# Optimization experiments

Hardware: AMD Instinct MI355X
Metric: run time of the kernel (lower is better)

The kernel has to match this reference:

```python
import jax, jax.numpy as jnp
import numpy as np

B, S, D = 1, 2048, 2048
H, DH, DHID, DKER = 16, 128, 128, 64
EPS = 1e-6

def _gelu(x):
    return jax.nn.gelu(x, approximate=False)  # torch F.gelu default is exact erf

def setup_inputs() -> dict:
    key = jax.random.key(0)
    ks = jax.random.split(key, 12)
    inp = {
        'q': jax.random.normal(ks[0], (B, S, D), jnp.float32),
        'k': jax.random.normal(ks[1], (B, S, D), jnp.float32),
        'v': jax.random.normal(ks[2], (B, S, D), jnp.float32),
        'lr_attn_mask': jax.random.randint(ks[3], (1, 1, S, S), 0, 2) > 0,
        'sparse_norms_lse': jax.random.normal(ks[4], (B, H, S, 1), jnp.float32),
        'sparse_attn_weights': jax.random.normal(ks[5], (B, H, S, S), jnp.float32) * 0.1,
        'kernel_q_mat1': jax.random.normal(ks[6], (H, DH, DHID), jnp.float32) * 0.05,
        'kernel_k_mat1': jax.random.normal(ks[7], (H, DH, DHID), jnp.float32) * 0.05,
        'kernel_q_mat2': jax.random.normal(ks[8], (H, DHID, DKER), jnp.float32) * 0.05,
        'kernel_k_mat2': jax.random.normal(ks[9], (H, DHID, DKER), jnp.float32) * 0.05,
        'interaction_k': jax.random.normal(ks[10], (H, DKER, DKER), jnp.float32) * 0.05,
        'scalingD': jnp.ones((1, H, 1, DKER), jnp.float32) * 1e-4,
        'scalingD2': jnp.ones((1, H, 1, DKER), jnp.float32) * 1e-4,
    }
    return inp

def reference(q, k, v, lr_attn_mask, sparse_norms_lse, sparse_attn_weights,
              kernel_q_mat1, kernel_k_mat1, kernel_q_mat2, kernel_k_mat2,
              interaction_k, scalingD, scalingD2):
    b, s, d = q.shape
    dh = d // H
    # [B,S,D] -> [B,H,S,dh]
    q = q.reshape(b, s, H, dh).transpose(0, 2, 1, 3)
    k = k.reshape(b, s, H, dh).transpose(0, 2, 1, 3)
    v = v.reshape(b, s, H, dh).transpose(0, 2, 1, 3)
    # per-head kernel feature maps (dropout is identity, p=0.0)
    q = _gelu(jnp.einsum('bhsd,hde->bhse', q, kernel_q_mat1))
    q = _gelu(jnp.einsum('bhsd,hde->bhse', q, kernel_q_mat2))
    k = _gelu(jnp.einsum('bhsd,hde->bhse', k, kernel_k_mat1))
    k = jnp.abs(scalingD) * _gelu(jnp.einsum('bhsd,hde->bhse', k, kernel_k_mat2))
    k = k + jnp.einsum('bhse,hef->bhsf', k, interaction_k) * scalingD2
    # low-rank kernelized scores: [B,H,S,S]
    out = jnp.einsum('bhse,bhte->bhst', jnp.abs(q), jnp.abs(k))
    mask = lr_attn_mask  # bool, broadcasts over [B,H,S,S]
    out = jnp.where(mask, out, 0.0)
    lr_norms_lse = jnp.log(out.sum(axis=-1, keepdims=True) + EPS)
    norm_factor_lse = jnp.logaddexp(lr_norms_lse, sparse_norms_lse)
    # log-domain merge of low-rank and sparse scores
    out = jnp.where(mask, jnp.log(out + EPS), sparse_attn_weights)
    out = jnp.exp(out - norm_factor_lse)
    out = jnp.einsum('bhst,bhtd->bhsd', out, v)
    return out.transpose(0, 2, 1, 3).reshape(b, s, d)
```

## Files before the change

kernel.cpp:

```cpp
#include <hip/hip_runtime.h>
#include <math.h>

#define S 2048
#define DD 2048
#define NH 16
#define DH 128
#define DHID 128
#define DKER 64
#define EPSF 1e-6f

typedef __attribute__((ext_vector_type(8))) short bf16x8;
typedef __attribute__((ext_vector_type(4))) float f32x4;

__device__ __forceinline__ float gelu_f(float x) {
    return 0.5f * x * (1.0f + erff(x * 0.7071067811865475f));
}

__device__ __forceinline__ ushort f2b(float x) {
    uint32_t u = __float_as_uint(x);
    uint32_t r = (u + 0x7FFFu + ((u >> 16) & 1u)) >> 16;
    return (ushort)r;
}

__global__ __launch_bounds__(256) void k_mlp1(const float* __restrict__ X,
                                              const float* __restrict__ Wall,
                                              float* __restrict__ Y) {
    const int h = blockIdx.y;
    const int s0 = blockIdx.x * 64;
    const int tid = threadIdx.x;
    const int ty = tid >> 4, tx = tid & 15;
    __shared__ float Xs[64][20];
    __shared__ float Ws[16][128];
    const float* Wh = Wall + h * DH * DHID;
    float acc[4][8] = {};

    const int lr = tid >> 2, lc = tid & 3;
    const int wr = tid >> 5, wc = tid & 31;
    for (int kc = 0; kc < 8; ++kc) {
        *(float4*)(&Xs[lr][lc * 4]) =
            *(const float4*)(X + (size_t)(s0 + lr) * DD + h * DH + kc * 16 + lc * 4);
        *(float4*)(&Ws[wr][wc * 4]) =
            *(const float4*)(Wh + (kc * 16 + wr) * DHID + wc * 4);
        *(float4*)(&Ws[wr + 8][wc * 4]) =
            *(const float4*)(Wh + (kc * 16 + wr + 8) * DHID + wc * 4);
        __syncthreads();
        #pragma unroll
        for (int kk = 0; kk < 16; ++kk) {
            float a[4];
            #pragma unroll
            for (int i = 0; i < 4; ++i) a[i] = Xs[ty * 4 + i][kk];
            float4 b0 = *(const float4*)(&Ws[kk][tx * 8]);
            float4 b1 = *(const float4*)(&Ws[kk][tx * 8 + 4]);
            #pragma unroll
            for (int i = 0; i < 4; ++i) {
                acc[i][0] += a[i] * b0.x; acc[i][1] += a[i] * b0.y;
                acc[i][2] += a[i] * b0.z; acc[i][3] += a[i] * b0.w;
                acc[i][4] += a[i] * b1.x; acc[i][5] += a[i] * b1.y;
                acc[i][6] += a[i] * b1.z; acc[i][7] += a[i] * b1.w;
            }
        }
        __syncthreads();
    }
    float* Yp = Y + ((size_t)h * S + s0) * DHID;
    #pragma unroll
    for (int i = 0; i < 4; ++i) {
        float4 o0, o1;
        o0.x = gelu_f(acc[i][0]); o0.y = gelu_f(acc[i][1]);
        o0.z = gelu_f(acc[i][2]); o0.w = gelu_f(acc[i][3]);
        o1.x = gelu_f(acc[i][4]); o1.y = gelu_f(acc[i][5]);
        o1.z = gelu_f(acc[i][6]); o1.w = gelu_f(acc[i][7]);
        *(float4*)(Yp + (ty * 4 + i) * DHID + tx * 8) = o0;
        *(float4*)(Yp + (ty * 4 + i) * DHID + tx * 8 + 4) = o1;
    }
}

__global__ __launch_bounds__(256) void k_mlp2_q(const float* __restrict__ Y1,
                                                const float* __restrict__ Wall,
                                                ushort* __restrict__ Q2) {
    const int h = blockIdx.y;
    const int s0 = blockIdx.x * 64;
    const int tid = threadIdx.x;
    const int ty = tid >> 4, tx = tid & 15;
    __shared__ float Ys[64][20];
    __shared__ float Ws[16][64];
    const float* Wh = Wall + h * DHID * DKER;
    float acc[4][4] = {};
    const int lr = tid >> 2, lc = tid & 3;
    const int wr = tid >> 4, wc = tid & 15;
    for (int kc = 0; kc < 8; ++kc) {
        *(float4*)(&Ys[lr][lc * 4]) =
            *(const float4*)(Y1 + ((size_t)h * S + s0 + lr) * DHID + kc * 16 + lc * 4);
        *(float4*)(&Ws[wr][wc * 4]) =
            *(const float4*)(Wh + (kc * 16 + wr) * DKER + wc * 4);
        __syncthreads();
        #pragma unroll
        for (int kk = 0; kk < 16; ++kk) {
            float4 b = *(const float4*)(&Ws[kk][tx * 4]);
            #pragma unroll
            for (int i = 0; i < 4; ++i) {
                float a = Ys[ty * 4 + i][kk];
                acc[i][0] += a * b.x; acc[i][1] += a * b.y;
                acc[i][2] += a * b.z; acc[i][3] += a * b.w;
            }
        }
        __syncthreads();
    }
    ushort* Qp = Q2 + ((size_t)h * S + s0) * DKER;
    #pragma unroll
    for (int i = 0; i < 4; ++i) {
        ushort4 o;
        o.x = f2b(fabsf(gelu_f(acc[i][0]))); o.y = f2b(fabsf(gelu_f(acc[i][1])));
        o.z = f2b(fabsf(gelu_f(acc[i][2]))); o.w = f2b(fabsf(gelu_f(acc[i][3])));
        *(ushort4*)(Qp + (ty * 4 + i) * DKER + tx * 4) = o;
    }
}

__global__ __launch_bounds__(256) void k_mlp2_k(const float* __restrict__ Y1,
                                                const float* __restrict__ Wall,
                                                const float* __restrict__ Ikall,
                                                const float* __restrict__ sD,
                                                const float* __restrict__ sD2,
                                                ushort* __restrict__ K3) {
    const int h = blockIdx.y;
    const int s0 = blockIdx.x * 64;
    const int tid = threadIdx.x;
    const int ty = tid >> 4, tx = tid & 15;
    __shared__ float Ys[64][20];
    __shared__ float Ws[16][64];
    __shared__ float K2s[64][68];
    __shared__ float Iks[64][64];
    const float* Wh = Wall + h * DHID * DKER;
    const float* Ikh = Ikall + h * DKER * DKER;
    #pragma unroll
    for (int it = 0; it < 4; ++it) {
        int idx = it * 256 + tid;
        int r = idx >> 4, c = idx & 15;
        *(float4*)(&Iks[r][c * 4]) = *(const float4*)(Ikh + r * DKER + c * 4);
    }
    float acc[4][4] = {};
    const int lr = tid >> 2, lc = tid & 3;
    const int wr = tid >> 4, wc = tid & 15;
    for (int kc = 0; kc < 8; ++kc) {
        *(float4*)(&Ys[lr][lc * 4]) =
            *(const float4*)(Y1 + ((size_t)h * S + s0 + lr) * DHID + kc * 16 + lc * 4);
        *(float4*)(&Ws[wr][wc * 4]) =
            *(const float4*)(Wh + (kc * 16 + wr) * DKER + wc * 4);
        __syncthreads();
        #pragma unroll
        for (int kk = 0; kk < 16; ++kk) {
            float4 b = *(const float4*)(&Ws[kk][tx * 4]);
            #pragma unroll
            for (int i = 0; i < 4; ++i) {
                float a = Ys[ty * 4 + i][kk];
                acc[i][0] += a * b.x; acc[i][1] += a * b.y;
                acc[i][2] += a * b.z; acc[i][3] += a * b.w;
            }
        }
        __syncthreads();
    }
    float sdv[4], sd2v[4];
    #pragma unroll
    for (int j = 0; j < 4; ++j) {
        sdv[j] = fabsf(sD[h * DKER + tx * 4 + j]);
        sd2v[j] = sD2[h * DKER + tx * 4 + j];
    }
    float k2r[4][4];
    #pragma unroll
    for (int i = 0; i < 4; ++i) {
        #pragma unroll
        for (int j = 0; j < 4; ++j) k2r[i][j] = sdv[j] * gelu_f(acc[i][j]);
        float4 o; o.x = k2r[i][0]; o.y = k2r[i][1]; o.z = k2r[i][2]; o.w = k2r[i][3];
        *(float4*)(&K2s[ty * 4 + i][tx * 4]) = o;
    }
    __syncthreads();
    float acc2[4][4] = {};
    #pragma unroll 16
    for (int f = 0; f < 64; ++f) {
        float4 b = *(const float4*)(&Iks[f][tx * 4]);
        #pragma unroll
        for (int i = 0; i < 4; ++i) {
            float a = K2s[ty * 4 + i][f];
            acc2[i][0] += a * b.x; acc2[i][1] += a * b.y;
            acc2[i][2] += a * b.z; acc2[i][3] += a * b.w;
        }
    }
    ushort* Kp = K3 + ((size_t)h * S + s0) * DKER;
    #pragma unroll
    for (int i = 0; i < 4; ++i) {
        ushort4 o;
        o.x = f2b(fabsf(k2r[i][0] + acc2[i][0] * sd2v[0]));
        o.y = f2b(fabsf(k2r[i][1] + acc2[i][1] * sd2v[1]));
        o.z = f2b(fabsf(k2r[i][2] + acc2[i][2] * sd2v[2]));
        o.w = f2b(fabsf(k2r[i][3] + acc2[i][3] * sd2v[3]));
        *(ushort4*)(Kp + (ty * 4 + i) * DKER + tx * 4) = o;
    }
}

__global__ __launch_bounds__(256) void k_vt(const float* __restrict__ V,
                                            ushort* __restrict__ Vt) {
    const int h = blockIdx.y;
    const int t0 = blockIdx.x * 64;
    const int tid = threadIdx.x;
    __shared__ ushort Ls[128][72];
    #pragma unroll
    for (int it = 0; it < 8; ++it) {
        int idx = it * 256 + tid;
        int r = idx >> 5, c4 = idx & 31;
        float4 v = *(const float4*)(V + (size_t)(t0 + r) * DD + h * DH + c4 * 4);
        Ls[c4 * 4 + 0][r] = f2b(v.x);
        Ls[c4 * 4 + 1][r] = f2b(v.y);
        Ls[c4 * 4 + 2][r] = f2b(v.z);
        Ls[c4 * 4 + 3][r] = f2b(v.w);
    }
    __syncthreads();
    #pragma unroll
    for (int it = 0; it < 4; ++it) {
        int idx = it * 256 + tid;
        int row = idx >> 3, cc = idx & 7;
        *(bf16x8*)(Vt + ((size_t)h * DH + row) * S + t0 + cc * 8) =
            *(const bf16x8*)(&Ls[row][cc * 8]);
    }
}

__global__ __launch_bounds__(256) void k_attn(const ushort* __restrict__ Q2,
                                              const ushort* __restrict__ K3,
                                              const ushort* __restrict__ Vt,
                                              const int* __restrict__ mask,
                                              const float* __restrict__ Wsp,
                                              const float* __restrict__ lse,
                                              float* __restrict__ out) {
    const int h = blockIdx.y;
    const int s0 = blockIdx.x * 64;
    const int tid = threadIdx.x;
    const int wv = tid >> 6;
    const int lane = tid & 63;
    const int ln = lane & 15;
    const int quad = lane >> 4;
    __shared__ ushort Q2s[64][72];
    __shared__ ushort K3s[64][72];
    __shared__ ushort Vts[128][72];
    __shared__ ushort Ps[4][16][72];

    #pragma unroll
    for (int it = 0; it < 2; ++it) {
        int idx = it * 256 + tid;
        int r = idx >> 3, c = idx & 7;
        *(bf16x8*)&Q2s[r][c * 8] =
            *(const bf16x8*)(Q2 + ((size_t)h * S + s0 + r) * DKER + c * 8);
    }

    f32x4 O[8];
    #pragma unroll
    for (int v = 0; v < 8; ++v) O[v] = (f32x4){0.f, 0.f, 0.f, 0.f};
    float rs[4] = {0.f, 0.f, 0.f, 0.f};
    const int srow_q = s0 + wv * 16 + quad * 4;

    for (int t0 = 0; t0 < S; t0 += 64) {
        __syncthreads();
        #pragma unroll
        for (int it = 0; it < 2; ++it) {
            int idx = it * 256 + tid;
            int r = idx >> 3, c = idx & 7;
            *(bf16x8*)&K3s[r][c * 8] =
                *(const bf16x8*)(K3 + ((size_t)h * S + t0 + r) * DKER + c * 8);
        }
        #pragma unroll
        for (int it = 0; it < 4; ++it) {
            int idx = it * 256 + tid;
            int r = idx >> 3, c = idx & 7;
            *(bf16x8*)&Vts[r][c * 8] =
                *(const bf16x8*)(Vt + ((size_t)h * DH + r) * S + t0 + c * 8);
        }
        int mk[4][4];
        float ww[4][4];
        #pragma unroll
        for (int n = 0; n < 4; ++n)
            #pragma unroll
            for (int r = 0; r < 4; ++r) {
                size_t off = (size_t)(srow_q + r) * S + t0 + n * 16 + ln;
                mk[n][r] = mask[off];
                ww[n][r] = Wsp[(size_t)h * S * S + off];
            }
        __syncthreads();

        f32x4 sc[4];
        #pragma unroll
        for (int n = 0; n < 4; ++n) sc[n] = (f32x4){0.f, 0.f, 0.f, 0.f};
        #pragma unroll
        for (int ks = 0; ks < 2; ++ks) {
            bf16x8 af = *(const bf16x8*)&Q2s[wv * 16 + ln][ks * 32 + quad * 8];
            #pragma unroll
            for (int n = 0; n < 4; ++n) {
                bf16x8 bf = *(const bf16x8*)&K3s[n * 16 + ln][ks * 32 + quad * 8];
                sc[n] = __builtin_amdgcn_mfma_f32_16x16x32_bf16(af, bf, sc[n], 0, 0, 0);
            }
        }
        #pragma unroll
        for (int n = 0; n < 4; ++n)
            #pragma unroll
            for (int r = 0; r < 4; ++r) {
                float s = sc[n][r];
                float p;
                if (mk[n][r]) { rs[r] += s; p = s + EPSF; }
                else          { p = expf(ww[n][r]); }
                Ps[wv][quad * 4 + r][n * 16 + ln] = f2b(p);
            }
        #pragma unroll
        for (int ks = 0; ks < 2; ++ks) {
            bf16x8 pf = *(const bf16x8*)&Ps[wv][ln][ks * 32 + quad * 8];
            #pragma unroll
            for (int v = 0; v < 8; ++v) {
                bf16x8 vf = *(const bf16x8*)&Vts[v * 16 + ln][ks * 32 + quad * 8];
                O[v] = __builtin_amdgcn_mfma_f32_16x16x32_bf16(pf, vf, O[v], 0, 0, 0);
            }
        }
    }
    #pragma unroll
    for (int r = 0; r < 4; ++r) {
        float v = rs[r];
        v += __shfl_xor(v, 1); v += __shfl_xor(v, 2);
        v += __shfl_xor(v, 4); v += __shfl_xor(v, 8);
        rs[r] = v;
    }
    float idv[4];
    #pragma unroll
    for (int r = 0; r < 4; ++r)
        idv[r] = 1.f / (rs[r] + EPSF + expf(lse[(size_t)h * S + srow_q + r]));
    #pragma unroll
    for (int v = 0; v < 8; ++v)
        #pragma unroll
        for (int r = 0; r < 4; ++r)
            out[(size_t)(srow_q + r) * DD + h * DH + v * 16 + ln] = O[v][r] * idv[r];
}

extern "C" void kernel_launch(void* const* d_in, const int* in_sizes, int n_in,
                              void* d_out, int out_size, void* d_ws, size_t ws_size,
                              hipStream_t stream) {
    const float* q   = (const float*)d_in[0];
    const float* k   = (const float*)d_in[1];
    const float* v   = (const float*)d_in[2];
    const int*   msk = (const int*)d_in[3];
    const float* lse = (const float*)d_in[4];
    const float* spw = (const float*)d_in[5];
    const float* wq1 = (const float*)d_in[6];
    const float* wk1 = (const float*)d_in[7];
    const float* wq2 = (const float*)d_in[8];
    const float* wk2 = (const float*)d_in[9];
    const float* ik  = (const float*)d_in[10];
    const float* sD  = (const float*)d_in[11];
    const float* sD2 = (const float*)d_in[12];
    float* out = (float*)d_out;

    float* ws = (float*)d_ws;
    float*  q1  = ws;
    float*  k1  = q1 + (size_t)NH * S * DHID;
    ushort* q2b = (ushort*)(k1 + (size_t)NH * S * DHID);
    ushort* k3b = q2b + (size_t)NH * S * DKER;
    ushort* vt  = k3b + (size_t)NH * S * DKER;

    dim3 g(S / 64, NH), b(256);
    k_mlp1<<<g, b, 0, stream>>>(q, wq1, q1);
    k_mlp1<<<g, b, 0, stream>>>(k, wk1, k1);
    k_mlp2_q<<<g, b, 0, stream>>>(q1, wq2, q2b);
    k_mlp2_k<<<g, b, 0, stream>>>(k1, wk2, ik, sD, sD2, k3b);
    k_vt<<<g, b, 0, stream>>>(v, vt);
    k_attn<<<g, b, 0, stream>>>(q2b, k3b, vt, msk, spw, lse, out);
}
```

Baseline: 564.9 us.

## Bit-pack attention mask and software-pipeline attention loop with register double buffering

Adds a pre-pass kernel that packs the int32 mask into bitwords via wave ballot, so the attention kernel reads 1 bit per element instead of 4 bytes per head. The attention kernel drops shared-memory staging of Q, K and V, loads MFMA fragments straight from global memory, and double-buffers K fragments, mask words and sparse weights across tiles to hide latency. It also swaps expf for __expf and sets launch bounds for two blocks per CU. The cost is more registers, redundant global reads of V across waves, and an extra kernel launch.

```diff
diff --git a/kernel.cpp b/kernel.cpp
--- a/kernel.cpp
+++ b/kernel.cpp
@@ -222,13 +222,25 @@
     }
 }
 
-__global__ __launch_bounds__(256) void k_attn(const ushort* __restrict__ Q2,
-                                              const ushort* __restrict__ K3,
-                                              const ushort* __restrict__ Vt,
-                                              const int* __restrict__ mask,
-                                              const float* __restrict__ Wsp,
-                                              const float* __restrict__ lse,
-                                              float* __restrict__ out) {
+__global__ __launch_bounds__(256) void k_mpack(const int* __restrict__ mask,
+                                               uint* __restrict__ pm) {
+    const int gw = blockIdx.x * 4 + (threadIdx.x >> 6);
+    const int lane = threadIdx.x & 63;
+    const int row = gw >> 5;
+    const int w64 = gw & 31;
+    int mv = mask[(size_t)row * S + w64 * 64 + lane];
+    unsigned long long b = __ballot(mv != 0);
+    if (lane == 0)  pm[row * 64 + w64 * 2]     = (uint)b;
+    if (lane == 32) pm[row * 64 + w64 * 2 + 1] = (uint)(b >> 32);
+}
+
+__global__ __launch_bounds__(256, 2) void k_attn(const ushort* __restrict__ Q2,
+                                                 const ushort* __restrict__ K3,
+                                                 const ushort* __restrict__ Vt,
+                                                 const uint* __restrict__ pm,
+                                                 const float* __restrict__ Wsp,
+                                                 const float* __restrict__ lse,
+                                                 float* __restrict__ out) {
     const int h = blockIdx.y;
     const int s0 = blockIdx.x * 64;
     const int tid = threadIdx.x;
@@ -236,85 +248,80 @@
     const int lane = tid & 63;
     const int ln = lane & 15;
     const int quad = lane >> 4;
-    __shared__ ushort Q2s[64][72];
-    __shared__ ushort K3s[64][72];
-    __shared__ ushort Vts[128][72];
     __shared__ ushort Ps[4][16][72];
 
-    #pragma unroll
-    for (int it = 0; it < 2; ++it) {
-        int idx = it * 256 + tid;
-        int r = idx >> 3, c = idx & 7;
-        *(bf16x8*)&Q2s[r][c * 8] =
-            *(const bf16x8*)(Q2 + ((size_t)h * S + s0 + r) * DKER + c * 8);
-    }
+    const ushort* K3h = K3 + (size_t)h * S * DKER;
+    const ushort* Vth = Vt + (size_t)h * DH * S;
+    const float*  Wh  = Wsp + (size_t)h * S * S;
+    const int srow_q = s0 + wv * 16 + quad * 4;
+
+    bf16x8 aq[2];
+    #pragma unroll
+    for (int ks = 0; ks < 2; ++ks)
+        aq[ks] = *(const bf16x8*)(Q2 + ((size_t)h * S + s0 + wv * 16 + ln) * DKER +
+                                  ks * 32 + quad * 8);
 
     f32x4 O[8];
     #pragma unroll
     for (int v = 0; v < 8; ++v) O[v] = (f32x4){0.f, 0.f, 0.f, 0.f};
     float rs[4] = {0.f, 0.f, 0.f, 0.f};
-    const int srow_q = s0 + wv * 16 + quad * 4;
-
-    for (int t0 = 0; t0 < S; t0 += 64) {
-        __syncthreads();
-        #pragma unroll
-        for (int it = 0; it < 2; ++it) {
-            int idx = it * 256 + tid;
-            int r = idx >> 3, c = idx & 7;
-            *(bf16x8*)&K3s[r][c * 8] =
-                *(const bf16x8*)(K3 + ((size_t)h * S + t0 + r) * DKER + c * 8);
-        }
-        #pragma unroll
-        for (int it = 0; it < 4; ++it) {
-            int idx = it * 256 + tid;
-            int r = idx >> 3, c = idx & 7;
-            *(bf16x8*)&Vts[r][c * 8] =
-                *(const bf16x8*)(Vt + ((size_t)h * DH + r) * S + t0 + c * 8);
-        }
-        int mk[4][4];
-        float ww[4][4];
-        #pragma unroll
-        for (int n = 0; n < 4; ++n)
-            #pragma unroll
-            for (int r = 0; r < 4; ++r) {
-                size_t off = (size_t)(srow_q + r) * S + t0 + n * 16 + ln;
-                mk[n][r] = mask[off];
-                ww[n][r] = Wsp[(size_t)h * S * S + off];
-            }
-        __syncthreads();
-
-        f32x4 sc[4];
-        #pragma unroll
-        for (int n = 0; n < 4; ++n) sc[n] = (f32x4){0.f, 0.f, 0.f, 0.f};
-        #pragma unroll
-        for (int ks = 0; ks < 2; ++ks) {
-            bf16x8 af = *(const bf16x8*)&Q2s[wv * 16 + ln][ks * 32 + quad * 8];
-            #pragma unroll
-            for (int n = 0; n < 4; ++n) {
-                bf16x8 bf = *(const bf16x8*)&K3s[n * 16 + ln][ks * 32 + quad * 8];
-                sc[n] = __builtin_amdgcn_mfma_f32_16x16x32_bf16(af, bf, sc[n], 0, 0, 0);
-            }
-        }
-        #pragma unroll
-        for (int n = 0; n < 4; ++n)
-            #pragma unroll
-            for (int r = 0; r < 4; ++r) {
-                float s = sc[n][r];
-                float p;
-                if (mk[n][r]) { rs[r] += s; p = s + EPSF; }
-                else          { p = expf(ww[n][r]); }
-                Ps[wv][quad * 4 + r][n * 16 + ln] = f2b(p);
-            }
-        #pragma unroll
-        for (int ks = 0; ks < 2; ++ks) {
-            bf16x8 pf = *(const bf16x8*)&Ps[wv][ln][ks * 32 + quad * 8];
-            #pragma unroll
-            for (int v = 0; v < 8; ++v) {
-                bf16x8 vf = *(const bf16x8*)&Vts[v * 16 + ln][ks * 32 + quad * 8];
-                O[v] = __builtin_amdgcn_mfma_f32_16x16x32_bf16(pf, vf, O[v], 0, 0, 0);
-            }
-        }
-    }
+
+    bf16x8 bk[2][2][4];
+    float  ww[2][4][4];
+    uint2  mw[2][4];
+
+#define ISSUE(TILE, P) do {                                                        \
+    const int t0_ = (TILE) * 64;                                                   \
+    _Pragma("unroll") for (int ks_ = 0; ks_ < 2; ++ks_)                            \
+    _Pragma("unroll") for (int n_ = 0; n_ < 4; ++n_)                               \
+        bk[P][ks_][n_] = *(const bf16x8*)(K3h +                                    \
+            (size_t)(t0_ + n_ * 16 + ln) * DKER + ks_ * 32 + quad * 8);            \
+    _Pragma("unroll") for (int r_ = 0; r_ < 4; ++r_)                               \
+        mw[P][r_] = *(const uint2*)(pm + (size_t)(srow_q + r_) * 64 + (t0_ >> 5)); \
+    _Pragma("unroll") for (int n_ = 0; n_ < 4; ++n_)                               \
+    _Pragma("unroll") for (int r_ = 0; r_ < 4; ++r_)                               \
+        ww[P][n_][r_] = Wh[(size_t)(srow_q + r_) * S + t0_ + n_ * 16 + ln];        \
+} while (0)
+
+#define COMPUTE(TILE, P) do {                                                      \
+    const int t0_ = (TILE) * 64;                                                   \
+    f32x4 sc[4];                                                                   \
+    _Pragma("unroll") for (int n_ = 0; n_ < 4; ++n_)                               \
+        sc[n_] = (f32x4){0.f, 0.f, 0.f, 0.f};                                      \
+    _Pragma("unroll") for (int ks_ = 0; ks_ < 2; ++ks_)                            \
+    _Pragma("unroll") for (int n_ = 0; n_ < 4; ++n_)                               \
+        sc[n_] = __builtin_amdgcn_mfma_f32_16x16x32_bf16(aq[ks_], bk[P][ks_][n_],  \
+                                                         sc[n_], 0, 0, 0);         \
+    _Pragma("unroll") for (int n_ = 0; n_ < 4; ++n_)                               \
+    _Pragma("unroll") for (int r_ = 0; r_ < 4; ++r_) {                             \
+        uint word = (n_ >= 2) ? mw[P][r_].y : mw[P][r_].x;                         \
+        int m_ = (word >> (((n_ & 1) << 4) + ln)) & 1;                             \
+        float s_ = sc[n_][r_];                                                     \
+        float p_;                                                                  \
+        if (m_) { rs[r_] += s_; p_ = s_ + EPSF; }                                  \
+        else    { p_ = __expf(ww[P][n_][r_]); }                                    \
+        Ps[wv][quad * 4 + r_][n_ * 16 + ln] = f2b(p_);                             \
+    }                                                                              \
+    _Pragma("unroll") for (int ks_ = 0; ks_ < 2; ++ks_) {                          \
+        bf16x8 pf = *(const bf16x8*)&Ps[wv][ln][ks_ * 32 + quad * 8];              \
+        _Pragma("unroll") for (int v_ = 0; v_ < 8; ++v_) {                         \
+            bf16x8 vf = *(const bf16x8*)(Vth + (size_t)(v_ * 16 + ln) * S + t0_ +  \
+                                         ks_ * 32 + quad * 8);                     \
+            O[v_] = __builtin_amdgcn_mfma_f32_16x16x32_bf16(pf, vf, O[v_], 0, 0, 0); \
+        }                                                                          \
+    }                                                                              \
+} while (0)
+
+    ISSUE(0, 0);
+    for (int it = 0; it < 32; it += 2) {
+        ISSUE(it + 1, 1);
+        COMPUTE(it, 0);
+        if (it + 2 < 32) ISSUE(it + 2, 0);
+        COMPUTE(it + 1, 1);
+    }
+#undef ISSUE
+#undef COMPUTE
+
     #pragma unroll
     for (int r = 0; r < 4; ++r) {
         float v = rs[r];
@@ -357,12 +364,14 @@
     ushort* q2b = (ushort*)(k1 + (size_t)NH * S * DHID);
     ushort* k3b = q2b + (size_t)NH * S * DKER;
     ushort* vt  = k3b + (size_t)NH * S * DKER;
+    uint*   pm  = (uint*)(vt + (size_t)NH * DH * S);
 
     dim3 g(S / 64, NH), b(256);
+    k_mpack<<<dim3(S * 32 / 4), b, 0, stream>>>(msk, pm);
     k_mlp1<<<g, b, 0, stream>>>(q, wq1, q1);
     k_mlp1<<<g, b, 0, stream>>>(k, wk1, k1);
     k_mlp2_q<<<g, b, 0, stream>>>(q1, wq2, q2b);
     k_mlp2_k<<<g, b, 0, stream>>>(k1, wk2, ik, sD, sD2, k3b);
     k_vt<<<g, b, 0, stream>>>(v, vt);
-    k_attn<<<g, b, 0, stream>>>(q2b, k3b, vt, msk, spw, lse, out);
-}
+    k_attn<<<g, b, 0, stream>>>(q2b, k3b, vt, pm, spw, lse, out);
+}
```

After: 625.3 us. 1.11x slower.
